# Optimization experiments

Hardware: AMD Instinct MI355X
Metric: run time of the kernel (lower is better)

The kernel has to match this reference:

```python
import jax, jax.numpy as jnp
import numpy as np

SCALE = 256.0
QMIN, QMAX = -32768.0, 32767.0
EPS = 1e-5
NUM_HEADS = 16

def fpq(t):
    return jnp.clip(jnp.round(t * SCALE), QMIN, QMAX) / SCALE

def layer_norm(x, g, b):
    mu = jnp.mean(x, axis=-1, keepdims=True)
    var = jnp.mean(jnp.square(x - mu), axis=-1, keepdims=True)
    return (x - mu) * jax.lax.rsqrt(var + EPS) * g + b

def setup_inputs() -> dict:
    key = jax.random.key(0)
    ks = jax.random.split(key, 10)
    B, S, D, H = 8, 1024, 1024, 4096
    s = 1.0 / np.sqrt(D)
    sh = 1.0 / np.sqrt(H)
    return {
        "x": jax.random.normal(ks[0], (B, S, D), jnp.float32),
        "Wqkv": jax.random.uniform(ks[1], (D, 3 * D), jnp.float32, -s, s),
        "bqkv": jax.random.uniform(ks[2], (3 * D,), jnp.float32, -s, s),
        "Wout": jax.random.uniform(ks[3], (D, D), jnp.float32, -s, s),
        "bout": jax.random.uniform(ks[4], (D,), jnp.float32, -s, s),
        "W1": jax.random.uniform(ks[5], (D, H), jnp.float32, -s, s),
        "b1": jax.random.uniform(ks[6], (H,), jnp.float32, -s, s),
        "W2": jax.random.uniform(ks[7], (H, D), jnp.float32, -sh, sh),
        "b2": jax.random.uniform(ks[8], (D,), jnp.float32, -sh, sh),
        "g1": jnp.ones((D,), jnp.float32),
        "beta1": jnp.zeros((D,), jnp.float32),
        "g2": jnp.ones((D,), jnp.float32),
        "beta2": jnp.zeros((D,), jnp.float32),
    }

def reference(x, Wqkv, bqkv, Wout, bout, W1, b1, W2, b2, g1, beta1, g2, beta2):
    B, S, D = x.shape
    Hh = NUM_HEADS
    hd = D // Hh
    # --- attention on norm1(x) ---
    xn = layer_norm(x, g1, beta1)
    qkv = fpq(xn @ Wqkv + bqkv)                       # [B,S,3D]
    q, k, v = jnp.split(qkv, 3, axis=-1)
    q = q.reshape(B, S, Hh, hd).transpose(0, 2, 1, 3)  # [B,H,S,hd]
    k = k.reshape(B, S, Hh, hd).transpose(0, 2, 1, 3)
    v = v.reshape(B, S, Hh, hd).transpose(0, 2, 1, 3)
    scores = jnp.einsum("bhqd,bhkd->bhqk", q, k) / np.sqrt(hd)
    probs = fpq(jax.nn.softmax(scores, axis=-1))
    ctx = jnp.einsum("bhqk,bhkd->bhqd", probs, v)
    ctx = ctx.transpose(0, 2, 1, 3).reshape(B, S, D)
    attn = fpq(ctx @ Wout + bout)
    x = fpq(x + fpq(attn))
    # --- MLP on norm2(x) ---
    xn2 = layer_norm(x, g2, beta2)
    h = jax.nn.relu(fpq(xn2 @ W1 + b1))
    mlp = fpq(h @ W2 + b2)
    x = fpq(x + fpq(mlp))
    return x
```

## Files before the change

kernel.cpp:

```cpp
#include <hip/hip_runtime.h>
#include <hip/hip_fp16.h>
#include <stdint.h>

typedef _Float16 f16;
typedef _Float16 f16x4 __attribute__((ext_vector_type(4)));
typedef _Float16 f16x8 __attribute__((ext_vector_type(8)));
typedef float f32x4 __attribute__((ext_vector_type(4)));

__device__ __forceinline__ float fpq(float t) {
    float r = rintf(t * 256.0f);
    r = fminf(fmaxf(r, -32768.0f), 32767.0f);
    return r * 0.00390625f;
}

__device__ __forceinline__ int swzkey(int r) { return (r & 3) | ((r >> 1) & 4); }

__device__ __forceinline__ void gll16(const f16* g, f16* l) {
    __builtin_amdgcn_global_load_lds(
        (const __attribute__((address_space(1))) uint32_t*)g,
        (__attribute__((address_space(3))) uint32_t*)l, 16, 0, 0);
}

template <int N> __device__ __forceinline__ void waitvm() {
    if constexpr (N == 0)      asm volatile("s_waitcnt vmcnt(0)" ::: "memory");
    else if constexpr (N == 1) asm volatile("s_waitcnt vmcnt(1)" ::: "memory");
    else if constexpr (N == 2) asm volatile("s_waitcnt vmcnt(2)" ::: "memory");
    else if constexpr (N == 4) asm volatile("s_waitcnt vmcnt(4)" ::: "memory");
    else if constexpr (N == 6) asm volatile("s_waitcnt vmcnt(6)" ::: "memory");
    else                       asm volatile("s_waitcnt vmcnt(8)" ::: "memory");
}

__device__ __forceinline__ void ln_body(
        const float* __restrict__ x, const float* __restrict__ g,
        const float* __restrict__ b, f16* __restrict__ out,
        int row, float* red) {
    int t = threadIdx.x;
    const float4* xr = (const float4*)(x + (size_t)row * 1024);
    float4 v = xr[t];
    float s = v.x + v.y + v.z + v.w;
    float s2 = v.x * v.x + v.y * v.y + v.z * v.z + v.w * v.w;
#pragma unroll
    for (int o = 32; o >= 1; o >>= 1) {
        s += __shfl_down(s, o);
        s2 += __shfl_down(s2, o);
    }
    int wid = t >> 6;
    if ((t & 63) == 0) { red[wid] = s; red[4 + wid] = s2; }
    __syncthreads();
    float ts = red[0] + red[1] + red[2] + red[3];
    float ts2 = red[4] + red[5] + red[6] + red[7];
    float mu = ts * (1.0f / 1024.0f);
    float var = ts2 * (1.0f / 1024.0f) - mu * mu;
    float rs = rsqrtf(var + 1e-5f);
    float4 gg = ((const float4*)g)[t];
    float4 bb = ((const float4*)b)[t];
    f16x4 o4;
    o4[0] = (f16)((v.x - mu) * rs * gg.x + bb.x);
    o4[1] = (f16)((v.y - mu) * rs * gg.y + bb.y);
    o4[2] = (f16)((v.z - mu) * rs * gg.z + bb.z);
    o4[3] = (f16)((v.w - mu) * rs * gg.w + bb.w);
    ((f16x4*)out)[(size_t)row * 256 + t] = o4;
}

__device__ __forceinline__ void tr_body(
        const float* __restrict__ W, f16* __restrict__ WT,
        int K, int N, int bx, int by, float* smem) {
    float (*tile)[33] = (float (*)[33])smem;
    int n0 = bx * 32, k0 = by * 32;
    int tx = threadIdx.x & 31, ty = threadIdx.x >> 5;
#pragma unroll
    for (int i = 0; i < 32; i += 8)
        tile[ty + i][tx] = W[(size_t)(k0 + ty + i) * N + n0 + tx];
    __syncthreads();
#pragma unroll
    for (int i = 0; i < 32; i += 8)
        WT[(size_t)(n0 + ty + i) * K + k0 + tx] = (f16)tile[tx][ty + i];
}

__global__ __launch_bounds__(256) void prologue_kernel(
        const float* __restrict__ x, const float* __restrict__ g1,
        const float* __restrict__ b1, f16* __restrict__ xn,
        const float* __restrict__ Wqkv, f16* __restrict__ wqkvT,
        const float* __restrict__ Wout, f16* __restrict__ woutT) {
    __shared__ float smem[32 * 33];
    int id = blockIdx.x;
    if (id < 8192) {
        ln_body(x, g1, b1, xn, id, smem);
    } else if (id < 8192 + 3072) {
        int q = id - 8192;
        tr_body(Wqkv, wqkvT, 1024, 3072, q % 96, q / 96, smem);
    } else {
        int q = id - (8192 + 3072);
        tr_body(Wout, woutT, 1024, 1024, q % 32, q / 32, smem);
    }
}

__global__ __launch_bounds__(256) void midlogue_kernel(
        const float* __restrict__ x1, const float* __restrict__ g2,
        const float* __restrict__ b2, f16* __restrict__ xn,
        const float* __restrict__ W1, f16* __restrict__ w1T,
        const float* __restrict__ W2, f16* __restrict__ w2T) {
    __shared__ float smem[32 * 33];
    int id = blockIdx.x;
    if (id < 8192) {
        ln_body(x1, g2, b2, xn, id, smem);
    } else if (id < 8192 + 4096) {
        int q = id - 8192;
        tr_body(W1, w1T, 1024, 4096, q % 128, q / 128, smem);
    } else {
        int q = id - (8192 + 4096);
        tr_body(W2, w2T, 4096, 1024, q % 32, q / 32, smem);
    }
}

__global__ __launch_bounds__(256) void transpose_kernel(
        const float* __restrict__ W, f16* __restrict__ WT, int K, int N) {
    __shared__ float smem[32 * 33];
    tr_body(W, WT, K, N, blockIdx.x, blockIdx.y, smem);
}

template <int EPI>
__global__ __launch_bounds__(256, 2) void gemmd_kernel(
        const f16* __restrict__ A, const f16* __restrict__ BT,
        int N, int K, int GM, int GN,
        const float* __restrict__ bias, const float* __restrict__ resid,
        void* __restrict__ out0, f16* __restrict__ outk, f16* __restrict__ outv) {
    constexpr int ABUF = 128 * 64;
    constexpr int BUFSZ = 2 * ABUF;
    __shared__ f16 lds[2 * BUFSZ];

    int nwg = GM * GN;
    int orig = blockIdx.x;
    int wg = (orig & 7) * (nwg >> 3) + (orig >> 3);
    int st = wg >> 6, in = wg & 63;
    int bm = (st % (GM >> 3)) * 8 + (in >> 3);
    int bn = (st / (GM >> 3)) * 8 + (in & 7);
    int m0 = bm * 128, n0 = bn * 128;
    int tid = threadIdx.x;
    int lane = tid & 63;
    int lr = lane & 15, lg = lane >> 4;
    int wv = tid >> 6;
    int wm = wv >> 1, wn = wv & 1;

    size_t srcA[4], srcB[4]; int dst[4];
#pragma unroll
    for (int j = 0; j < 4; ++j) {
        int row = j * 32 + (tid >> 3);
        int slot = (tid & 7) ^ (row & 7);
        srcA[j] = (size_t)(m0 + row) * K + slot * 8;
        srcB[j] = (size_t)(n0 + row) * K + slot * 8;
        dst[j] = j * 2048 + tid * 8;
    }

    int offA[2][4], offB[4][2];
#pragma unroll
    for (int i = 0; i < 4; ++i) {
        int row = wm * 64 + i * 16 + lr;
#pragma unroll
        for (int kk = 0; kk < 2; ++kk)
            offA[kk][i] = row * 64 + (((kk * 4 + lg) ^ (row & 7)) * 8);
    }
#pragma unroll
    for (int j = 0; j < 4; ++j) {
        int n = wn * 64 + j * 16 + lr;
#pragma unroll
        for (int kk = 0; kk < 2; ++kk)
            offB[j][kk] = ABUF + n * 64 + (((kk * 4 + lg) ^ (n & 7)) * 8);
    }

    f32x4 acc[4][4] = {};
    int NT = K >> 6;

#pragma unroll
    for (int j = 0; j < 4; ++j) gll16(A + srcA[j], lds + dst[j]);
#pragma unroll
    for (int j = 0; j < 4; ++j) gll16(BT + srcB[j], lds + ABUF + dst[j]);
#pragma unroll
    for (int j = 0; j < 4; ++j) gll16(A + srcA[j] + 64, lds + BUFSZ + dst[j]);
#pragma unroll
    for (int j = 0; j < 4; ++j) gll16(BT + srcB[j] + 64, lds + BUFSZ + ABUF + dst[j]);
    waitvm<8>();
    __builtin_amdgcn_s_barrier();
    __builtin_amdgcn_sched_barrier(0);

    for (int t = 0; t < NT; ++t) {
        int cur = t & 1;
        f16* Ab = lds + cur * BUFSZ;
        f16x8 a0[4], a1[4], b00, b01, b10, b11;
#pragma unroll
        for (int i = 0; i < 4; ++i) a0[i] = *(const f16x8*)&Ab[offA[0][i]];
        b00 = *(const f16x8*)&Ab[offB[0][0]];
        b01 = *(const f16x8*)&Ab[offB[1][0]];
#pragma unroll
        for (int i = 0; i < 4; ++i) a1[i] = *(const f16x8*)&Ab[offA[1][i]];
        b10 = *(const f16x8*)&Ab[offB[0][1]];
        b11 = *(const f16x8*)&Ab[offB[1][1]];
        __builtin_amdgcn_s_setprio(1);
#pragma unroll
        for (int i = 0; i < 4; ++i) {
            acc[i][0] = __builtin_amdgcn_mfma_f32_16x16x32_f16(a0[i], b00, acc[i][0], 0, 0, 0);
            acc[i][1] = __builtin_amdgcn_mfma_f32_16x16x32_f16(a0[i], b01, acc[i][1], 0, 0, 0);
        }
#pragma unroll
        for (int i = 0; i < 4; ++i) {
            acc[i][0] = __builtin_amdgcn_mfma_f32_16x16x32_f16(a1[i], b10, acc[i][0], 0, 0, 0);
            acc[i][1] = __builtin_amdgcn_mfma_f32_16x16x32_f16(a1[i], b11, acc[i][1], 0, 0, 0);
        }
        __builtin_amdgcn_s_setprio(0);
        f16x8 b20 = *(const f16x8*)&Ab[offB[2][0]];
        f16x8 b30 = *(const f16x8*)&Ab[offB[3][0]];
        f16x8 b21 = *(const f16x8*)&Ab[offB[2][1]];
        f16x8 b31 = *(const f16x8*)&Ab[offB[3][1]];
        asm volatile("s_waitcnt lgkmcnt(0)" ::: "memory");
        __builtin_amdgcn_sched_barrier(0);
        __builtin_amdgcn_s_barrier();
        if (t + 2 < NT) {
            size_t kof = (size_t)(t + 2) << 6;
#pragma unroll
            for (int j = 0; j < 4; ++j) gll16(A + srcA[j] + kof, Ab + dst[j]);
#pragma unroll
            for (int j = 0; j < 4; ++j) gll16(BT + srcB[j] + kof, Ab + ABUF + dst[j]);
        }
        __builtin_amdgcn_s_setprio(1);
#pragma unroll
        for (int i = 0; i < 4; ++i) {
            acc[i][2] = __builtin_amdgcn_mfma_f32_16x16x32_f16(a0[i], b20, acc[i][2], 0, 0, 0);
            acc[i][3] = __builtin_amdgcn_mfma_f32_16x16x32_f16(a0[i], b30, acc[i][3], 0, 0, 0);
        }
#pragma unroll
        for (int i = 0; i < 4; ++i) {
            acc[i][2] = __builtin_amdgcn_mfma_f32_16x16x32_f16(a1[i], b21, acc[i][2], 0, 0, 0);
            acc[i][3] = __builtin_amdgcn_mfma_f32_16x16x32_f16(a1[i], b31, acc[i][3], 0, 0, 0);
        }
        __builtin_amdgcn_s_setprio(0);
        if (t + 2 < NT) { waitvm<8>(); }
        else if (t + 1 < NT) { waitvm<0>(); }
        __builtin_amdgcn_sched_barrier(0);
        __builtin_amdgcn_s_barrier();
    }

#pragma unroll
    for (int i = 0; i < 4; ++i) {
#pragma unroll
        for (int j = 0; j < 4; ++j) {
            int col = n0 + wn * 64 + j * 16 + lr;
            float bv = bias[col];
#pragma unroll
            for (int r = 0; r < 4; ++r) {
                int row = m0 + wm * 64 + i * 16 + lg * 4 + r;
                float val = acc[i][j][r] + bv;
                if (EPI == 0) {
                    float qv = fpq(val);
                    int part = col >> 10, wi = col & 1023;
                    int hd = wi >> 6, d = wi & 63;
                    int bb = row >> 10, ss = row & 1023;
                    size_t bh = (size_t)(bb * 16 + hd);
                    if (part == 0) {
                        ((f16*)out0)[(bh * 1024 + ss) * 64 + d] = (f16)qv;
                    } else if (part == 1) {
                        outk[bh * 65536 + (ss >> 6) * 4096 + (ss & 63) * 64 + (d ^ (swzkey(ss) << 3))] = (f16)qv;
                    } else {
                        outv[bh * 65536 + (ss >> 6) * 4096 + d * 64 + ((ss & 63) ^ (swzkey(d) << 3))] = (f16)qv;
                    }
                } else if (EPI == 2) {
                    float hv = fmaxf(fpq(val), 0.0f);
                    ((f16*)out0)[(size_t)row * N + col] = (f16)hv;
                } else {
                    float o = fpq(resid[(size_t)row * 1024 + col] + fpq(val));
                    ((float*)out0)[(size_t)row * 1024 + col] = o;
                }
            }
        }
    }
}

__global__ __launch_bounds__(512) void attn_kernel(
        const f16* __restrict__ Q, const f16* __restrict__ Kg,
        const f16* __restrict__ Vt, f16* __restrict__ ctx) {
    int id = blockIdx.x;
    int qt = (id >> 3) & 7;
    int bh = (id >> 6) * 8 + (id & 7);
    int b = bh >> 4, h = bh & 15;
    const f16* Qp = Q + ((size_t)bh * 1024 + (size_t)qt * 128) * 64;
    const f16* Kp = Kg + (size_t)bh * 65536;
    const f16* Vp = Vt + (size_t)bh * 65536;
    int t = threadIdx.x, lane = t & 63, w = t >> 6;
    int lr = lane & 15, lg = lane >> 4;
    __shared__ f16 Ks[2][4096];
    __shared__ f16 Vs[2][4096];
    int so = t * 8;

    const float L2E = 1.4426950408889634f;
    const float C0 = -24.0f * 1.4426950408889634f;

    f16x8 qf[2];
#pragma unroll
    for (int kk = 0; kk < 2; ++kk) {
        qf[kk] = *(const f16x8*)(Qp + (w * 16 + lr) * 64 + kk * 32 + lg * 8);
#pragma unroll
        for (int j = 0; j < 8; ++j) qf[kk][j] = qf[kk][j] * (f16)0.125f;
    }
    int koff[4][2], voff[4][2];
#pragma unroll
    for (int nf = 0; nf < 4; ++nf) {
        int rowv = 32 * (nf >> 1) + 8 * ((lr >> 2) ^ (2 * (nf & 1))) + 4 * (nf & 1) + (lr & 3);
#pragma unroll
        for (int kk = 0; kk < 2; ++kk)
            koff[nf][kk] = rowv * 64 + (((kk * 4 + lg) ^ swzkey(rowv)) * 8);
    }
#pragma unroll
    for (int db = 0; db < 4; ++db) {
        int d = db * 16 + lr;
#pragma unroll
        for (int kk = 0; kk < 2; ++kk)
            voff[db][kk] = d * 64 + (((kk * 4 + lg) ^ swzkey(d)) * 8);
    }

    gll16(Kp + so, Ks[0] + so);
    float lsum = 0.0f;
    for (int kt = 0; kt < 16; ++kt) {
        int cur = kt & 1;
        if (kt < 15) {
            gll16(Kp + (kt + 1) * 4096 + so, Ks[cur ^ 1] + so);
            waitvm<1>();
        } else {
            waitvm<0>();
        }
        __builtin_amdgcn_sched_barrier(0);
        __builtin_amdgcn_s_barrier();
        f32x4 sc[4] = {};
#pragma unroll
        for (int kk = 0; kk < 2; ++kk)
#pragma unroll
            for (int nf = 0; nf < 4; ++nf) {
                f16x8 kf = *(const f16x8*)&Ks[cur][koff[nf][kk]];
                sc[nf] = __builtin_amdgcn_mfma_f32_16x16x32_f16(kf, qf[kk], sc[nf], 0, 0, 0);
            }
        float part = 0.0f;
#pragma unroll
        for (int nf = 0; nf < 4; ++nf)
#pragma unroll
            for (int r = 0; r < 4; ++r)
                part += __builtin_amdgcn_exp2f(fmaf(sc[nf][r], L2E, C0));
        lsum += part;
        __builtin_amdgcn_s_barrier();
    }
    lsum += __shfl_xor(lsum, 16);
    lsum += __shfl_xor(lsum, 32);
    float rl256 = 256.0f * __builtin_amdgcn_rcpf(lsum);

    f32x4 co[4] = {};
    const float inv256 = 0.00390625f;
    gll16(Kp + so, Ks[0] + so);
    gll16(Vp + so, Vs[0] + so);
    for (int kt = 0; kt < 16; ++kt) {
        int cur = kt & 1;
        if (kt < 15) {
            gll16(Kp + (kt + 1) * 4096 + so, Ks[cur ^ 1] + so);
            gll16(Vp + (kt + 1) * 4096 + so, Vs[cur ^ 1] + so);
            waitvm<2>();
        } else {
            waitvm<0>();
        }
        __builtin_amdgcn_sched_barrier(0);
        __builtin_amdgcn_s_barrier();
        f32x4 sc[4] = {};
#pragma unroll
        for (int kk = 0; kk < 2; ++kk)
#pragma unroll
            for (int nf = 0; nf < 4; ++nf) {
                f16x8 kf = *(const f16x8*)&Ks[cur][koff[nf][kk]];
                sc[nf] = __builtin_amdgcn_mfma_f32_16x16x32_f16(kf, qf[kk], sc[nf], 0, 0, 0);
            }
        uint32_t pk0[4], pk1[4];
#pragma unroll
        for (int nf = 0; nf < 4; ++nf) {
            float e0 = __builtin_amdgcn_exp2f(fmaf(sc[nf][0], L2E, C0));
            float e1 = __builtin_amdgcn_exp2f(fmaf(sc[nf][1], L2E, C0));
            float e2 = __builtin_amdgcn_exp2f(fmaf(sc[nf][2], L2E, C0));
            float e3 = __builtin_amdgcn_exp2f(fmaf(sc[nf][3], L2E, C0));
            float r0 = rintf(e0 * rl256);
            float r1 = rintf(e1 * rl256);
            float r2 = rintf(e2 * rl256);
            float r3 = rintf(e3 * rl256);
            pk0[nf] = __builtin_bit_cast(uint32_t,
                        __builtin_amdgcn_cvt_pkrtz(r0 * inv256, r1 * inv256));
            pk1[nf] = __builtin_bit_cast(uint32_t,
                        __builtin_amdgcn_cvt_pkrtz(r2 * inv256, r3 * inv256));
        }
#pragma unroll
        for (int kk = 0; kk < 2; ++kk) {
            uint4 fw;
            fw.x = pk0[2 * kk];
            fw.y = pk1[2 * kk];
            fw.z = __shfl_xor(pk0[2 * kk + 1], 32);
            fw.w = __shfl_xor(pk1[2 * kk + 1], 32);
            f16x8 pa = __builtin_bit_cast(f16x8, fw);
#pragma unroll
            for (int db = 0; db < 4; ++db) {
                f16x8 vb = *(const f16x8*)&Vs[cur][voff[db][kk]];
                co[db] = __builtin_amdgcn_mfma_f32_16x16x32_f16(pa, vb, co[db], 0, 0, 0);
            }
        }
        __builtin_amdgcn_s_barrier();
    }
#pragma unroll
    for (int db = 0; db < 4; ++db)
#pragma unroll
        for (int r = 0; r < 4; ++r) {
            int ss = qt * 128 + w * 16 + lg * 4 + r;
            ctx[((size_t)b * 1024 + ss) * 1024 + h * 64 + db * 16 + lr] = (f16)co[db][r];
        }
}

extern "C" void kernel_launch(void* const* d_in, const int* in_sizes, int n_in,
                              void* d_out, int out_size, void* d_ws, size_t ws_size,
                              hipStream_t stream) {
    const float* x     = (const float*)d_in[0];
    const float* Wqkv  = (const float*)d_in[1];
    const float* bqkv  = (const float*)d_in[2];
    const float* Wout  = (const float*)d_in[3];
    const float* bout  = (const float*)d_in[4];
    const float* W1    = (const float*)d_in[5];
    const float* b1    = (const float*)d_in[6];
    const float* W2    = (const float*)d_in[7];
    const float* b2    = (const float*)d_in[8];
    const float* g1    = (const float*)d_in[9];
    const float* beta1 = (const float*)d_in[10];
    const float* g2    = (const float*)d_in[11];
    const float* beta2 = (const float*)d_in[12];

    char* ws = (char*)d_ws;
    const size_t MB = 1ull << 20;
    f16*  q_h    = (f16*)(ws);
    f16*  k_h    = (f16*)(ws + 16 * MB);
    f16*  vt_h   = (f16*)(ws + 32 * MB);
    f16*  ctx_h  = (f16*)(ws + 48 * MB);
    f16*  h_h    = (f16*)(ws);
    f16*  xn_h   = (f16*)(ws + 64 * MB);
    float* x1    = (float*)(ws + 80 * MB);
    f16*  wqkvT  = (f16*)(ws + 112 * MB);
    f16*  woutT  = (f16*)(ws + 118 * MB);
    f16*  w1T    = (f16*)(ws + 112 * MB);
    bool bigws   = ws_size >= (size_t)130 * MB;
    f16*  w2T    = bigws ? (f16*)(ws + 120 * MB) : (f16*)(ws + 112 * MB);

    prologue_kernel<<<8192 + 3072 + 1024, 256, 0, stream>>>(
        x, g1, beta1, xn_h, Wqkv, wqkvT, Wout, woutT);
    gemmd_kernel<0><<<1536, 256, 0, stream>>>(xn_h, wqkvT, 3072, 1024, 64, 24, bqkv, nullptr, q_h, k_h, vt_h);
    attn_kernel<<<1024, 512, 0, stream>>>(q_h, k_h, vt_h, ctx_h);
    gemmd_kernel<1><<<512, 256, 0, stream>>>(ctx_h, woutT, 1024, 1024, 64, 8, bout, x, x1, nullptr, nullptr);
    midlogue_kernel<<<bigws ? (8192 + 4096 + 4096) : (8192 + 4096), 256, 0, stream>>>(
        x1, g2, beta2, xn_h, W1, w1T, W2, w2T);
    gemmd_kernel<2><<<2048, 256, 0, stream>>>(xn_h, w1T, 4096, 1024, 64, 32, b1, nullptr, h_h, nullptr, nullptr);
    if (!bigws)
        transpose_kernel<<<dim3(32, 128), 256, 0, stream>>>(W2, w2T, 4096, 1024);
    gemmd_kernel<3><<<512, 256, 0, stream>>>(h_h, w2T, 1024, 4096, 64, 8, b2, x1, d_out, nullptr, nullptr);
}
```

Baseline: 352.1 us.

## Store intermediate residual in f16 and hoist all weight transposes to prologue

The post-attention residual x1 is now written and read as f16 instead of fp32, cutting its memory traffic in the out-proj epilogue, the second layernorm, and the final residual add. All four weight transposes move into one prologue launch with a fixed workspace layout, replacing the midlogue kernel and the conditional separate W2 transpose with a lean ln2 kernel. This risks precision loss for residual values whose magnitude exceeds the range where f16 can exactly represent 1/256 steps.

```diff
diff --git a/kernel.cpp b/kernel.cpp
--- a/kernel.cpp
+++ b/kernel.cpp
@@ -30,15 +30,13 @@
     else                       asm volatile("s_waitcnt vmcnt(8)" ::: "memory");
 }
 
-__device__ __forceinline__ void ln_body(
-        const float* __restrict__ x, const float* __restrict__ g,
-        const float* __restrict__ b, f16* __restrict__ out,
-        int row, float* red) {
+__device__ __forceinline__ void ln_core(
+        float v0, float v1, float v2, float v3,
+        const float* __restrict__ g, const float* __restrict__ b,
+        f16* __restrict__ out, int row, float* red) {
     int t = threadIdx.x;
-    const float4* xr = (const float4*)(x + (size_t)row * 1024);
-    float4 v = xr[t];
-    float s = v.x + v.y + v.z + v.w;
-    float s2 = v.x * v.x + v.y * v.y + v.z * v.z + v.w * v.w;
+    float s = v0 + v1 + v2 + v3;
+    float s2 = v0 * v0 + v1 * v1 + v2 * v2 + v3 * v3;
 #pragma unroll
     for (int o = 32; o >= 1; o >>= 1) {
         s += __shfl_down(s, o);
@@ -55,10 +53,10 @@
     float4 gg = ((const float4*)g)[t];
     float4 bb = ((const float4*)b)[t];
     f16x4 o4;
-    o4[0] = (f16)((v.x - mu) * rs * gg.x + bb.x);
-    o4[1] = (f16)((v.y - mu) * rs * gg.y + bb.y);
-    o4[2] = (f16)((v.z - mu) * rs * gg.z + bb.z);
-    o4[3] = (f16)((v.w - mu) * rs * gg.w + bb.w);
+    o4[0] = (f16)((v0 - mu) * rs * gg.x + bb.x);
+    o4[1] = (f16)((v1 - mu) * rs * gg.y + bb.y);
+    o4[2] = (f16)((v2 - mu) * rs * gg.z + bb.z);
+    o4[3] = (f16)((v3 - mu) * rs * gg.w + bb.w);
     ((f16x4*)out)[(size_t)row * 256 + t] = o4;
 }
 
@@ -81,42 +79,37 @@
         const float* __restrict__ x, const float* __restrict__ g1,
         const float* __restrict__ b1, f16* __restrict__ xn,
         const float* __restrict__ Wqkv, f16* __restrict__ wqkvT,
-        const float* __restrict__ Wout, f16* __restrict__ woutT) {
-    __shared__ float smem[32 * 33];
-    int id = blockIdx.x;
-    if (id < 8192) {
-        ln_body(x, g1, b1, xn, id, smem);
-    } else if (id < 8192 + 3072) {
-        int q = id - 8192;
-        tr_body(Wqkv, wqkvT, 1024, 3072, q % 96, q / 96, smem);
-    } else {
-        int q = id - (8192 + 3072);
-        tr_body(Wout, woutT, 1024, 1024, q % 32, q / 32, smem);
-    }
-}
-
-__global__ __launch_bounds__(256) void midlogue_kernel(
-        const float* __restrict__ x1, const float* __restrict__ g2,
-        const float* __restrict__ b2, f16* __restrict__ xn,
+        const float* __restrict__ Wout, f16* __restrict__ woutT,
         const float* __restrict__ W1, f16* __restrict__ w1T,
         const float* __restrict__ W2, f16* __restrict__ w2T) {
     __shared__ float smem[32 * 33];
     int id = blockIdx.x;
     if (id < 8192) {
-        ln_body(x1, g2, b2, xn, id, smem);
-    } else if (id < 8192 + 4096) {
+        const float4 v = ((const float4*)(x + (size_t)id * 1024))[threadIdx.x];
+        ln_core(v.x, v.y, v.z, v.w, g1, b1, xn, id, smem);
+    } else if (id < 8192 + 3072) {
         int q = id - 8192;
+        tr_body(Wqkv, wqkvT, 1024, 3072, q % 96, q / 96, smem);
+    } else if (id < 8192 + 3072 + 1024) {
+        int q = id - (8192 + 3072);
+        tr_body(Wout, woutT, 1024, 1024, q % 32, q / 32, smem);
+    } else if (id < 8192 + 3072 + 1024 + 4096) {
+        int q = id - (8192 + 3072 + 1024);
         tr_body(W1, w1T, 1024, 4096, q % 128, q / 128, smem);
     } else {
-        int q = id - (8192 + 4096);
+        int q = id - (8192 + 3072 + 1024 + 4096);
         tr_body(W2, w2T, 4096, 1024, q % 32, q / 32, smem);
     }
 }
 
-__global__ __launch_bounds__(256) void transpose_kernel(
-        const float* __restrict__ W, f16* __restrict__ WT, int K, int N) {
-    __shared__ float smem[32 * 33];
-    tr_body(W, WT, K, N, blockIdx.x, blockIdx.y, smem);
+__global__ __launch_bounds__(256) void ln2_kernel(
+        const f16* __restrict__ x, const float* __restrict__ g,
+        const float* __restrict__ b, f16* __restrict__ out) {
+    __shared__ float smem[8];
+    int row = blockIdx.x;
+    f16x4 v4 = ((const f16x4*)(x + (size_t)row * 1024))[threadIdx.x];
+    ln_core((float)v4[0], (float)v4[1], (float)v4[2], (float)v4[3],
+            g, b, out, row, smem);
 }
 
 template <int EPI>
@@ -124,6 +117,7 @@
         const f16* __restrict__ A, const f16* __restrict__ BT,
         int N, int K, int GM, int GN,
         const float* __restrict__ bias, const float* __restrict__ resid,
+        const f16* __restrict__ residh,
         void* __restrict__ out0, f16* __restrict__ outk, f16* __restrict__ outv) {
     constexpr int ABUF = 128 * 64;
     constexpr int BUFSZ = 2 * ABUF;
@@ -262,11 +256,14 @@
                     } else {
                         outv[bh * 65536 + (ss >> 6) * 4096 + d * 64 + ((ss & 63) ^ (swzkey(d) << 3))] = (f16)qv;
                     }
+                } else if (EPI == 1) {
+                    float o = fpq(resid[(size_t)row * 1024 + col] + fpq(val));
+                    ((f16*)out0)[(size_t)row * 1024 + col] = (f16)o;
                 } else if (EPI == 2) {
                     float hv = fmaxf(fpq(val), 0.0f);
                     ((f16*)out0)[(size_t)row * N + col] = (f16)hv;
                 } else {
-                    float o = fpq(resid[(size_t)row * 1024 + col] + fpq(val));
+                    float o = fpq((float)residh[(size_t)row * 1024 + col] + fpq(val));
                     ((float*)out0)[(size_t)row * 1024 + col] = o;
                 }
             }
@@ -438,22 +435,18 @@
     f16*  ctx_h  = (f16*)(ws + 48 * MB);
     f16*  h_h    = (f16*)(ws);
     f16*  xn_h   = (f16*)(ws + 64 * MB);
-    float* x1    = (float*)(ws + 80 * MB);
+    f16*  x1h    = (f16*)(ws + 80 * MB);
+    f16*  w1T    = (f16*)(ws + 96 * MB);
+    f16*  w2T    = (f16*)(ws + 104 * MB);
     f16*  wqkvT  = (f16*)(ws + 112 * MB);
     f16*  woutT  = (f16*)(ws + 118 * MB);
-    f16*  w1T    = (f16*)(ws + 112 * MB);
-    bool bigws   = ws_size >= (size_t)130 * MB;
-    f16*  w2T    = bigws ? (f16*)(ws + 120 * MB) : (f16*)(ws + 112 * MB);
-
-    prologue_kernel<<<8192 + 3072 + 1024, 256, 0, stream>>>(
-        x, g1, beta1, xn_h, Wqkv, wqkvT, Wout, woutT);
-    gemmd_kernel<0><<<1536, 256, 0, stream>>>(xn_h, wqkvT, 3072, 1024, 64, 24, bqkv, nullptr, q_h, k_h, vt_h);
+
+    prologue_kernel<<<8192 + 3072 + 1024 + 4096 + 4096, 256, 0, stream>>>(
+        x, g1, beta1, xn_h, Wqkv, wqkvT, Wout, woutT, W1, w1T, W2, w2T);
+    gemmd_kernel<0><<<1536, 256, 0, stream>>>(xn_h, wqkvT, 3072, 1024, 64, 24, bqkv, nullptr, nullptr, q_h, k_h, vt_h);
     attn_kernel<<<1024, 512, 0, stream>>>(q_h, k_h, vt_h, ctx_h);
-    gemmd_kernel<1><<<512, 256, 0, stream>>>(ctx_h, woutT, 1024, 1024, 64, 8, bout, x, x1, nullptr, nullptr);
-    midlogue_kernel<<<bigws ? (8192 + 4096 + 4096) : (8192 + 4096), 256, 0, stream>>>(
-        x1, g2, beta2, xn_h, W1, w1T, W2, w2T);
-    gemmd_kernel<2><<<2048, 256, 0, stream>>>(xn_h, w1T, 4096, 1024, 64, 32, b1, nullptr, h_h, nullptr, nullptr);
-    if (!bigws)
-        transpose_kernel<<<dim3(32, 128), 256, 0, stream>>>(W2, w2T, 4096, 1024);
-    gemmd_kernel<3><<<512, 256, 0, stream>>>(h_h, w2T, 1024, 4096, 64, 8, b2, x1, d_out, nullptr, nullptr);
-}
+    gemmd_kernel<1><<<512, 256, 0, stream>>>(ctx_h, woutT, 1024, 1024, 64, 8, bout, x, nullptr, x1h, nullptr, nullptr);
+    ln2_kernel<<<8192, 256, 0, stream>>>(x1h, g2, beta2, xn_h);
+    gemmd_kernel<2><<<2048, 256, 0, stream>>>(xn_h, w1T, 4096, 1024, 64, 32, b1, nullptr, nullptr, h_h, nullptr, nullptr);
+    gemmd_kernel<3><<<512, 256, 0, stream>>>(h_h, w2T, 1024, 4096, 64, 8, b2, nullptr, x1h, d_out, nullptr, nullptr);
+}
```

After: 350.9 us. Within noise of the previous version (-0.3%).
